# Optimization experiments

Hardware: AMD Instinct MI355X
Metric: run time of the kernel (lower is better)

Reference implementation:

```python
import jax, jax.numpy as jnp
import numpy as np

LEVEL_SHAPES = ((100, 100), (50, 50), (25, 25))  # (H, W) per feature level
B, S, D, H, L, P, FFN = 2, 13125, 256, 8, 3, 4, 1024
Dh = D // H


def setup_inputs() -> dict:
    key = jax.random.key(0)
    ks = jax.random.split(key, 24)

    def rn(k, shape, s=0.02):
        return jax.random.normal(k, shape, jnp.float32) * s

    starts = np.cumsum([0] + [h * w for h, w in LEVEL_SHAPES])[:-1]
    return {
        "x": jax.random.normal(ks[0], (B, S, D), jnp.float32),
        "pos_embed": jax.random.normal(ks[1], (B, S, D), jnp.float32) * 0.1,
        "ref_points": jax.random.uniform(ks[2], (B, S, L, 2), jnp.float32),
        "W_off": rn(ks[3], (D, H * L * P * 2)),
        "b_off": rn(ks[4], (H * L * P * 2,), 0.5),
        "W_attn": rn(ks[5], (D, H * L * P)),
        "b_attn": rn(ks[6], (H * L * P,)),
        "W_val": rn(ks[7], (D, D)),
        "b_val": rn(ks[8], (D,)),
        "W_out": rn(ks[9], (D, D)),
        "b_out": rn(ks[10], (D,)),
        "g1": jnp.ones((D,), jnp.float32),
        "be1": jnp.zeros((D,), jnp.float32),
        "W1": rn(ks[11], (D, FFN)),
        "b1": rn(ks[12], (FFN,)),
        "W2": rn(ks[13], (FFN, D)),
        "b2": rn(ks[14], (D,)),
        "g2": jnp.ones((D,), jnp.float32),
        "be2": jnp.zeros((D,), jnp.float32),
        "level_shapes": jnp.array(LEVEL_SHAPES, jnp.int32),
        "level_start_idx": jnp.array(starts, jnp.int32),
    }


def layer_norm(x, g, b, eps=1e-5):
    m = jnp.mean(x, -1, keepdims=True)
    v = jnp.var(x, -1, keepdims=True)
    return (x - m) * jax.lax.rsqrt(v + eps) * g + b


def bilinear_sample(vl, loc, Hl, Wl):
    # vl: [B,H,S_l,Dh]; loc: [B,H,S,P,2] normalized (x,y) in [0,1]
    # grid_sample semantics: align_corners=False, padding_mode='zeros'
    x = loc[..., 0] * Wl - 0.5
    y = loc[..., 1] * Hl - 0.5
    x0 = jnp.floor(x)
    y0 = jnp.floor(y)
    fx = x - x0
    fy = y - y0
    x0i = x0.astype(jnp.int32)
    y0i = y0.astype(jnp.int32)
    out = 0.0
    for dy, dx, w in ((0, 0, (1 - fx) * (1 - fy)), (0, 1, fx * (1 - fy)),
                      (1, 0, (1 - fx) * fy), (1, 1, fx * fy)):
        xi = x0i + dx
        yi = y0i + dy
        valid = (xi >= 0) & (xi < Wl) & (yi >= 0) & (yi < Hl)
        idx = jnp.clip(yi, 0, Hl - 1) * Wl + jnp.clip(xi, 0, Wl - 1)
        b_, h_, s_, p_ = idx.shape
        g = jnp.take_along_axis(vl, idx.reshape(b_, h_, s_ * p_)[..., None], axis=2)
        g = g.reshape(b_, h_, s_, p_, Dh)
        out = out + g * (w * valid)[..., None]
    return out  # [B,H,S,P,Dh]


def ms_deform_attn(q, x, ref_points, W_off, b_off, W_attn, b_attn, W_val, b_val, W_out, b_out):
    value = (x @ W_val + b_val).reshape(B, S, H, Dh).transpose(0, 2, 1, 3)  # [B,H,S,Dh]
    off = (q @ W_off + b_off).reshape(B, S, H, L, P, 2)
    attn = jax.nn.softmax((q @ W_attn + b_attn).reshape(B, S, H, L * P), axis=-1)
    attn = attn.reshape(B, S, H, L, P).transpose(0, 2, 1, 3, 4)  # [B,H,S,L,P]
    # offset normalizer is (W, H) per level
    norm = jnp.array([[w, h] for h, w in LEVEL_SHAPES], jnp.float32)
    loc = ref_points[:, :, None, :, None, :] + off / norm[None, None, None, :, None, :]
    loc = loc.transpose(0, 2, 1, 3, 4, 5)  # [B,H,S,L,P,2]
    s0 = 0
    sampled = []
    for l, (Hl, Wl) in enumerate(LEVEL_SHAPES):
        vl = jax.lax.slice_in_dim(value, s0, s0 + Hl * Wl, axis=2)
        sampled.append(bilinear_sample(vl, loc[:, :, :, l], Hl, Wl))
        s0 += Hl * Wl
    sampled = jnp.stack(sampled, axis=3)  # [B,H,S,L,P,Dh]
    out = jnp.einsum('bhslp,bhslpd->bshd', attn, sampled).reshape(B, S, D)
    return out @ W_out + b_out


def reference(x, pos_embed, ref_points, W_off, b_off, W_attn, b_attn, W_val, b_val,
              W_out, b_out, g1, be1, W1, b1, W2, b2, g2, be2,
              level_shapes, level_start_idx):
    q = x + pos_embed
    attn_out = ms_deform_attn(q, x, ref_points, W_off, b_off, W_attn, b_attn,
                              W_val, b_val, W_out, b_out)
    h1 = layer_norm(x + attn_out, g1, be1)
    ffn = jax.nn.relu(h1 @ W1 + b1) @ W2 + b2
    return layer_norm(h1 + ffn, g2, be2)
```

## Files before the change

### kernel.cpp

```cpp
#include <hip/hip_runtime.h>
#include <hip/hip_bf16.h>

namespace {

constexpr int kB = 2, kS = 13125, kD = 256, kH = 8, kL = 3, kP = 4, kFFN = 1024, kDh = 32;
constexpr int kM = kB * kS;

typedef __attribute__((ext_vector_type(8))) short short8v;
typedef __attribute__((ext_vector_type(4))) float f32x4;
typedef __attribute__((ext_vector_type(2))) float f32x2;
typedef __attribute__((ext_vector_type(2))) unsigned int uint2v;

__device__ __forceinline__ float bf2f(unsigned short u) {
  unsigned int x = ((unsigned int)u) << 16;
  return __builtin_bit_cast(float, x);
}
__device__ __forceinline__ unsigned short f2bf(float f) {
  unsigned int u = __builtin_bit_cast(unsigned int, f);
  u += 0x7FFFu + ((u >> 16) & 1u);
  return (unsigned short)(u >> 16);
}

__device__ __forceinline__ void gload_lds16(const void* g, void* l) {
  __builtin_amdgcn_global_load_lds(
      (const __attribute__((address_space(1))) unsigned int*)g,
      (__attribute__((address_space(3))) unsigned int*)l, 16, 0, 0);
}

__global__ __launch_bounds__(256) void wprep_kernel(const float* __restrict__ W,
                                                    unsigned short* __restrict__ Wt,
                                                    int K, int N, int total) {
  int idx = blockIdx.x * 256 + threadIdx.x;
  if (idx >= total) return;
  int n = idx / K, k = idx - n * K;
  float v = (n < N) ? W[(size_t)k * N + n] : 0.f;
  Wt[idx] = f2bf(v);
}

__global__ __launch_bounds__(256) void wprep_comb(const float* __restrict__ Woff,
                                                  const float* __restrict__ Wattn,
                                                  const float* __restrict__ boff,
                                                  const float* __restrict__ battn,
                                                  unsigned short* __restrict__ Wt,
                                                  float* __restrict__ bc) {
  int idx = blockIdx.x * 256 + threadIdx.x;
  if (idx >= 288 * 256) return;
  int n = idx >> 8, k = idx & 255;
  int h = n / 36, j = n - h * 36;
  float v = (j < 24) ? Woff[(size_t)k * 192 + h * 24 + j]
                     : Wattn[(size_t)k * 96 + h * 12 + (j - 24)];
  Wt[idx] = f2bf(v);
  if (idx < 288) {
    int hh = idx / 36, jj = idx - hh * 36;
    bc[idx] = (jj < 24) ? boff[hh * 24 + jj] : battn[hh * 12 + (jj - 24)];
  }
}

__global__ __launch_bounds__(256) void prep_kernel(const float4* __restrict__ x,
                                                   const float4* __restrict__ pos,
                                                   ushort4* __restrict__ xb,
                                                   ushort4* __restrict__ qb, int n4) {
  int i = blockIdx.x * 256 + threadIdx.x;
  if (i < n4) {
    float4 a = x[i], b = pos[i];
    xb[i] = make_ushort4(f2bf(a.x), f2bf(a.y), f2bf(a.z), f2bf(a.w));
    qb[i] = make_ushort4(f2bf(a.x + b.x), f2bf(a.y + b.y),
                         f2bf(a.z + b.z), f2bf(a.w + b.w));
  }
}

template <int EPI, bool OBF, int MI, bool VHM>
__global__ __launch_bounds__(256) void mfma_gemm(const unsigned short* __restrict__ A,
                                                 const unsigned short* __restrict__ Bt,
                                                 const float* __restrict__ bias,
                                                 void* __restrict__ Cp,
                                                 int M, int N, int K) {
  constexpr int BM = MI * 32;
  __shared__ unsigned short smem[2 * 128 * 32];
  unsigned short* As = smem;
  unsigned short* Bs = smem + BM * 32;
  const int tid = threadIdx.x;
  const int w = tid >> 6, lane = tid & 63;
  const int m0 = blockIdx.y * BM, n0 = blockIdx.x * 128;
  const int wr = w >> 1, wc = w & 1;
  const int r_ = lane >> 2, sl = lane & 3;

  f32x4 acc[MI][4] = {};

  for (int k0 = 0; k0 < K; k0 += 32) {
#pragma unroll
    for (int i = 0; i < MI / 2; ++i) {
      const int row = i * 64 + w * 16 + r_;
      const int sg = sl ^ ((row >> 1) & 3);
      int arow = m0 + row;
      arow = arow < M ? arow : M - 1;
      gload_lds16(A + (size_t)arow * K + k0 + sg * 8, &As[(i * 64 + w * 16) * 32]);
    }
#pragma unroll
    for (int i = 0; i < 2; ++i) {
      const int row = i * 64 + w * 16 + r_;
      const int sg = sl ^ ((row >> 1) & 3);
      gload_lds16(Bt + (size_t)(n0 + row) * K + k0 + sg * 8, &Bs[(i * 64 + w * 16) * 32]);
    }
    __syncthreads();
    short8v a[MI], b[4];
#pragma unroll
    for (int mi = 0; mi < MI; ++mi) {
      const int row = wr * (MI * 16) + mi * 16 + (lane & 15);
      const int slot = (lane >> 4) ^ ((row >> 1) & 3);
      a[mi] = *(const short8v*)&As[row * 32 + slot * 8];
    }
#pragma unroll
    for (int ni = 0; ni < 4; ++ni) {
      const int row = wc * 64 + ni * 16 + (lane & 15);
      const int slot = (lane >> 4) ^ ((row >> 1) & 3);
      b[ni] = *(const short8v*)&Bs[row * 32 + slot * 8];
    }
#pragma unroll
    for (int mi = 0; mi < MI; ++mi)
#pragma unroll
      for (int ni = 0; ni < 4; ++ni)
        acc[mi][ni] = __builtin_amdgcn_mfma_f32_16x16x32_bf16(a[mi], b[ni], acc[mi][ni], 0, 0, 0);
    __syncthreads();
  }

  const int cr = lane >> 4, cc = lane & 15;
  if (OBF) {
    unsigned short* Cs = smem;
#pragma unroll
    for (int half = 0; half < MI / 2; ++half) {
      if (MI == 2 || wr == half) {
#pragma unroll
        for (int ni = 0; ni < 4; ++ni) {
          const int col = wc * 64 + ni * 16 + cc;
          const float bv = bias[n0 + col];
#pragma unroll
          for (int mi = 0; mi < MI; ++mi)
#pragma unroll
            for (int r = 0; r < 4; ++r) {
              const int loc = wr * (MI * 16) + mi * 16 + cr * 4 + r - half * 64;
              float v = acc[mi][ni][r] + bv;
              if (EPI == 2) v = fmaxf(v, 0.f);
              const int ch = (col >> 3) ^ (loc & 7);
              Cs[loc * 128 + ch * 8 + (col & 7)] = f2bf(v);
            }
        }
      }
      __syncthreads();
      const int lr = tid >> 4, lc = tid & 15;
#pragma unroll
      for (int pp = 0; pp < 4; ++pp) {
        const int loc = pp * 16 + lr;
        const int grow = m0 + half * 64 + loc;
        const short8v vv = *(const short8v*)&Cs[loc * 128 + ((lc ^ (loc & 7)) * 8)];
        if (grow < M) {
          if (VHM) {
            const int col = n0 + lc * 8;
            const int bb = grow >= kS ? 1 : 0;
            const int ss = grow - bb * kS;
            const int hh = col >> 5;
            *(short8v*)((unsigned short*)Cp +
                        (((size_t)(bb * kH + hh) * kS + ss) * kDh + (col & 31))) = vv;
          } else {
            *(short8v*)((unsigned short*)Cp + (size_t)grow * N + n0 + lc * 8) = vv;
          }
        }
      }
      __syncthreads();
    }
  } else {
#pragma unroll
    for (int ni = 0; ni < 4; ++ni) {
      const int col = n0 + wc * 64 + ni * 16 + cc;
      if (col >= N) continue;
      const float bv = bias[col];
#pragma unroll
      for (int mi = 0; mi < MI; ++mi) {
#pragma unroll
        for (int r = 0; r < 4; ++r) {
          const int row = m0 + wr * (MI * 16) + mi * 16 + cr * 4 + r;
          if (row >= M) continue;
          ((float*)Cp)[(size_t)row * N + col] = acc[mi][ni][r] + bv;
        }
      }
    }
  }
}

__global__ __launch_bounds__(256) void ffn_fused(const unsigned short* __restrict__ Ain,
                                                 const unsigned short* __restrict__ W1t,
                                                 const unsigned short* __restrict__ W2t,
                                                 const float* __restrict__ b1,
                                                 const float* __restrict__ b2,
                                                 unsigned short* __restrict__ Cp,
                                                 int M) {
  __shared__ unsigned short W1s[2][64 * 256];
  __shared__ unsigned short Ps[2 * 64 * 32];
  const int tid = threadIdx.x;
  const int w = tid >> 6, lane = tid & 63;
  const int m0 = blockIdx.x * 64;
  const int cr = lane >> 4, cc = lane & 15;

  short8v areg[8];
  {
    int grow = m0 + w * 16 + cc;
    grow = grow < M ? grow : M - 1;
    const unsigned short* ap = Ain + (size_t)grow * 256 + cr * 8;
#pragma unroll
    for (int kk = 0; kk < 8; ++kk) areg[kk] = *(const short8v*)(ap + kk * 32);
  }

  auto stage_w1 = [&](int jt, int buf) {
    const unsigned short* src = W1t + (size_t)jt * 64 * 256;
#pragma unroll
    for (int it = 0; it < 8; ++it) {
      const int idx = it * 256 + tid;
      const int kk = idx >> 8;
      const int row = (idx >> 2) & 63;
      const int sl = idx & 3;
      const int ssl = sl ^ ((row >> 1) & 3);
      gload_lds16(src + (size_t)row * 256 + kk * 32 + ssl * 8, &W1s[buf][idx * 8]);
    }
  };

  f32x4 acc[4][4] = {};

  stage_w1(0, 0);
  __syncthreads();

  for (int jt = 0; jt < 16; ++jt) {
    const int buf = jt & 1;
    if (jt < 15) stage_w1(jt + 1, buf ^ 1);

    f32x4 p1[4] = {};
#pragma unroll
    for (int kk = 0; kk < 8; ++kk) {
#pragma unroll
      for (int ni = 0; ni < 4; ++ni) {
        const int row = ni * 16 + cc;
        const short8v wv = *(const short8v*)
            &W1s[buf][kk * 2048 + row * 32 + ((cr ^ ((row >> 1) & 3)) * 8)];
        p1[ni] = __builtin_amdgcn_mfma_f32_16x16x32_bf16(wv, areg[kk], p1[ni], 0, 0, 0);
      }
    }
    {
      const int row = w * 16 + cc;
      const int rsw = (row >> 1) & 3;
#pragma unroll
      for (int ni = 0; ni < 4; ++ni) {
        const float4 bv = *(const float4*)&b1[jt * 64 + ni * 16 + cr * 4];
        const unsigned int u0 =
            (unsigned)f2bf(fmaxf(p1[ni][0] + bv.x, 0.f)) |
            ((unsigned)f2bf(fmaxf(p1[ni][1] + bv.y, 0.f)) << 16);
        const unsigned int u1 =
            (unsigned)f2bf(fmaxf(p1[ni][2] + bv.z, 0.f)) |
            ((unsigned)f2bf(fmaxf(p1[ni][3] + bv.w, 0.f)) << 16);
        const int kb = ni >> 1;
        const int slot = (ni & 1) * 2 + (cr >> 1);
        uint2v* dst = (uint2v*)&Ps[kb * 2048 + row * 32 + ((slot ^ rsw) * 8) + (cr & 1) * 4];
        *dst = (uint2v){u0, u1};
      }
    }
    __syncthreads();

#pragma unroll
    for (int kk2 = 0; kk2 < 2; ++kk2) {
      short8v pf[4];
#pragma unroll
      for (int mi = 0; mi < 4; ++mi) {
        const int row = mi * 16 + cc;
        pf[mi] = *(const short8v*)
            &Ps[kk2 * 2048 + row * 32 + ((cr ^ ((row >> 1) & 3)) * 8)];
      }
#pragma unroll
      for (int ni = 0; ni < 4; ++ni) {
        const int ncol = w * 64 + ni * 16 + cc;
        const short8v wv = *(const short8v*)(W2t + (size_t)ncol * 1024 + jt * 64 + kk2 * 32 + cr * 8);
#pragma unroll
        for (int mi = 0; mi < 4; ++mi)
          acc[mi][ni] = __builtin_amdgcn_mfma_f32_16x16x32_bf16(pf[mi], wv, acc[mi][ni], 0, 0, 0);
      }
    }
    __syncthreads();
  }

  unsigned short* Cs = &W1s[0][0];
#pragma unroll
  for (int ni = 0; ni < 4; ++ni) {
    const int col = w * 64 + ni * 16 + cc;
    const float bv = b2[col];
#pragma unroll
    for (int mi = 0; mi < 4; ++mi)
#pragma unroll
      for (int r = 0; r < 4; ++r) {
        const int row = mi * 16 + cr * 4 + r;
        const float v = acc[mi][ni][r] + bv;
        Cs[row * 256 + (((col >> 3) ^ (row & 7)) * 8) + (col & 7)] = f2bf(v);
      }
  }
  __syncthreads();
#pragma unroll
  for (int it = 0; it < 8; ++it) {
    const int row = it * 8 + (tid >> 5);
    const int grow = m0 + row;
    const int ch = tid & 31;
    const short8v vv = *(const short8v*)&Cs[row * 256 + ((ch ^ (row & 7)) * 8)];
    if (grow < M) *(short8v*)(Cp + (size_t)grow * 256 + ch * 8) = vv;
  }
}

__device__ __forceinline__ void acc2u(f32x2* acc, unsigned u, int i, float m) {
  f32x2 v;
  v.x = __builtin_bit_cast(float, u << 16);
  v.y = __builtin_bit_cast(float, u & 0xFFFF0000u);
  acc[i] += m * v;
}
__device__ __forceinline__ void acc_corner(f32x2* acc, uint4 q, float m) {
  acc2u(acc, q.x, 0, m);
  acc2u(acc, q.y, 1, m);
  acc2u(acc, q.z, 2, m);
  acc2u(acc, q.w, 3, m);
}

__global__ __launch_bounds__(256) void sample_kernel(const unsigned short* __restrict__ value,
                                                     const float* __restrict__ oa,
                                                     const float* __restrict__ refp,
                                                     unsigned short* __restrict__ out) {
  const int tid = threadIdx.x;
  const int sub = tid >> 2;
  const int lane = tid & 3;
  const int gi = blockIdx.x * 64 + sub;
  if (gi >= kB * kS * kH) return;
  const int h = gi & 7;
  const int bs = gi >> 3;
  const int b = (bs >= kS) ? 1 : 0;

  const float* op = oa + (size_t)bs * 288 + h * 36;
  const float* al = op + 24;
  float w[12];
  float mx = -1e30f;
#pragma unroll
  for (int i = 0; i < 12; ++i) { w[i] = al[i]; mx = fmaxf(mx, w[i]); }
  float sum = 0.f;
#pragma unroll
  for (int i = 0; i < 12; ++i) { w[i] = __expf(w[i] - mx); sum += w[i]; }
  const float inv = 1.f / sum;
#pragma unroll
  for (int i = 0; i < 12; ++i) w[i] *= inv;

  const float* rp = refp + (size_t)bs * (kL * 2);
  const unsigned short* vbase = value + ((size_t)(b * kH + h) * kS) * kDh + lane * 8;

  const int LH[3] = {100, 50, 25}, LW[3] = {100, 50, 25}, LS[3] = {0, 10000, 12500};
  f32x2 acc[4] = {};
#pragma unroll
  for (int l = 0; l < 3; ++l) {
    const int Wi = LW[l], Hi = LH[l];
    const float Wl = (float)Wi, Hl = (float)Hi;
    const float rxw = rp[l * 2 + 0] * Wl - 0.5f;
    const float ryh = rp[l * 2 + 1] * Hl - 0.5f;
    const unsigned short* lvl = vbase + (size_t)LS[l] * kDh;
#pragma unroll
    for (int p = 0; p < 4; ++p) {
      const float ox = op[l * 8 + p * 2 + 0], oy = op[l * 8 + p * 2 + 1];
      const float xf = rxw + ox;
      const float yf = ryh + oy;
      const float x0f = floorf(xf), y0f = floorf(yf);
      const float fx = xf - x0f, fy = yf - y0f;
      const int x0 = (int)x0f, y0 = (int)y0f;
      const int x1 = x0 + 1, y1 = y0 + 1;
      const bool vx0 = (unsigned)x0 < (unsigned)Wi;
      const bool vx1 = (unsigned)x1 < (unsigned)Wi;
      const bool vy0 = (unsigned)y0 < (unsigned)Hi;
      const bool vy1 = (unsigned)y1 < (unsigned)Hi;
      const int cx0 = min(max(x0, 0), Wi - 1), cx1 = min(max(x1, 0), Wi - 1);
      const int cy0 = min(max(y0, 0), Hi - 1), cy1 = min(max(y1, 0), Hi - 1);
      const float aw = w[l * 4 + p];
      const float ax = aw * fx, a0 = aw - ax;
      const float w00 = a0 - a0 * fy, w10 = a0 * fy;
      const float w01 = ax - ax * fy, w11 = ax * fy;
      const float m00 = (vx0 && vy0) ? w00 : 0.f;
      const float m01 = (vx1 && vy0) ? w01 : 0.f;
      const float m10 = (vx0 && vy1) ? w10 : 0.f;
      const float m11 = (vx1 && vy1) ? w11 : 0.f;
      const int ry0 = cy0 * Wi, ry1 = cy1 * Wi;
      const uint4 q00 = *(const uint4*)(lvl + (size_t)(ry0 + cx0) * kDh);
      const uint4 q01 = *(const uint4*)(lvl + (size_t)(ry0 + cx1) * kDh);
      const uint4 q10 = *(const uint4*)(lvl + (size_t)(ry1 + cx0) * kDh);
      const uint4 q11 = *(const uint4*)(lvl + (size_t)(ry1 + cx1) * kDh);
      acc_corner(acc, q00, m00);
      acc_corner(acc, q01, m01);
      acc_corner(acc, q10, m10);
      acc_corner(acc, q11, m11);
    }
  }
  unsigned short r[8];
#pragma unroll
  for (int i = 0; i < 4; ++i) {
    r[2 * i] = f2bf(acc[i].x);
    r[2 * i + 1] = f2bf(acc[i].y);
  }
  *(short8v*)(out + (size_t)bs * kD + h * kDh + lane * 8) = *(const short8v*)r;
}

template <int WB>
__global__ __launch_bounds__(256) void lnres_kernel(const float* __restrict__ X,
                                                    const unsigned short* __restrict__ Ab,
                                                    const float* __restrict__ g,
                                                    const float* __restrict__ be,
                                                    float* __restrict__ out,
                                                    unsigned short* __restrict__ outb,
                                                    int rows) {
  const int wid = threadIdx.x >> 6, lane = threadIdx.x & 63;
  const int row = blockIdx.x * 4 + wid;
  if (row >= rows) return;
  const float4 v = ((const float4*)(X + (size_t)row * kD))[lane];
  const ushort4 a4 = ((const ushort4*)(Ab + (size_t)row * kD))[lane];
  float4 t;
  t.x = v.x + bf2f(a4.x);
  t.y = v.y + bf2f(a4.y);
  t.z = v.z + bf2f(a4.z);
  t.w = v.w + bf2f(a4.w);
  float s = t.x + t.y + t.z + t.w;
  float sq = t.x * t.x + t.y * t.y + t.z * t.z + t.w * t.w;
#pragma unroll
  for (int o = 1; o < 64; o <<= 1) {
    s += __shfl_xor(s, o);
    sq += __shfl_xor(sq, o);
  }
  const float mean = s * (1.f / kD);
  const float var = sq * (1.f / kD) - mean * mean;
  const float rs = rsqrtf(var + 1e-5f);
  const float4 gg = ((const float4*)g)[lane];
  const float4 bb = ((const float4*)be)[lane];
  float4 o4;
  o4.x = (t.x - mean) * rs * gg.x + bb.x;
  o4.y = (t.y - mean) * rs * gg.y + bb.y;
  o4.z = (t.z - mean) * rs * gg.z + bb.z;
  o4.w = (t.w - mean) * rs * gg.w + bb.w;
  ((float4*)(out + (size_t)row * kD))[lane] = o4;
  if (WB) {
    ((ushort4*)(outb + (size_t)row * kD))[lane] =
        make_ushort4(f2bf(o4.x), f2bf(o4.y), f2bf(o4.z), f2bf(o4.w));
  }
}

}

extern "C" void kernel_launch(void* const* d_in, const int* in_sizes, int n_in,
                              void* d_out, int out_size, void* d_ws, size_t ws_size,
                              hipStream_t stream) {
  const float* x      = (const float*)d_in[0];
  const float* pos    = (const float*)d_in[1];
  const float* refp   = (const float*)d_in[2];
  const float* W_off  = (const float*)d_in[3];
  const float* b_off  = (const float*)d_in[4];
  const float* W_attn = (const float*)d_in[5];
  const float* b_attn = (const float*)d_in[6];
  const float* W_val  = (const float*)d_in[7];
  const float* b_val  = (const float*)d_in[8];
  const float* W_out  = (const float*)d_in[9];
  const float* b_out  = (const float*)d_in[10];
  const float* g1     = (const float*)d_in[11];
  const float* be1    = (const float*)d_in[12];
  const float* W1     = (const float*)d_in[13];
  const float* b1     = (const float*)d_in[14];
  const float* W2     = (const float*)d_in[15];
  const float* b2     = (const float*)d_in[16];
  const float* g2     = (const float*)d_in[17];
  const float* be2    = (const float*)d_in[18];
  float* outp = (float*)d_out;

  char* ws = (char*)d_ws;
  unsigned short* Wvt = (unsigned short*)(ws + 0);
  unsigned short* Wot = (unsigned short*)(ws + 131072);
  unsigned short* Wct = (unsigned short*)(ws + 262144);
  float* bcomb        = (float*)(ws + 262144 + 288 * 512);
  unsigned short* W1t = (unsigned short*)(ws + 458752);
  unsigned short* W2t = (unsigned short*)(ws + 983040);
  const size_t MDb = (size_t)kM * kD * 2;
  char* regA = ws + 1507328;
  char* regB = regA + MDb;
  char* regC = regB + MDb;
  char* regG = regC + 43680000;

  unsigned short* xb    = (unsigned short*)regA;
  unsigned short* aob   = (unsigned short*)regA;
  unsigned short* qb    = (unsigned short*)regB;
  unsigned short* f2b   = (unsigned short*)regB;
  unsigned short* value = (unsigned short*)regC;
  float* oa   = (float*)(regC + MDb);
  float* h1   = (float*)regC;
  unsigned short* h1b = (unsigned short*)(regC + (size_t)kM * kD * 4);
  unsigned short* sv  = (unsigned short*)regG;

  const dim3 blk(256);
  const int mt64 = (kM + 63) / 64;
  const int n4 = kM * kD / 4;

  wprep_kernel<<<(256 * 256 + 255) / 256, blk, 0, stream>>>(W_val, Wvt, 256, 256, 256 * 256);
  wprep_kernel<<<(256 * 256 + 255) / 256, blk, 0, stream>>>(W_out, Wot, 256, 256, 256 * 256);
  wprep_comb<<<288, blk, 0, stream>>>(W_off, W_attn, b_off, b_attn, Wct, bcomb);
  wprep_kernel<<<(1024 * 256 + 255) / 256, blk, 0, stream>>>(W1, W1t, 256, 1024, 1024 * 256);
  wprep_kernel<<<(256 * 1024 + 255) / 256, blk, 0, stream>>>(W2, W2t, 1024, 256, 256 * 1024);

  prep_kernel<<<(n4 + 255) / 256, blk, 0, stream>>>((const float4*)x, (const float4*)pos,
                                                    (ushort4*)xb, (ushort4*)qb, n4);
  mfma_gemm<0, true, 2, true><<<dim3(2, mt64), blk, 0, stream>>>(xb, Wvt, b_val, value,
                                                                 kM, 256, 256);
  mfma_gemm<0, false, 2, false><<<dim3(3, mt64), blk, 0, stream>>>(qb, Wct, bcomb, oa,
                                                                   kM, 288, 256);
  sample_kernel<<<(kB * kS * kH + 63) / 64, blk, 0, stream>>>(value, oa, refp, sv);
  mfma_gemm<0, true, 2, false><<<dim3(2, mt64), blk, 0, stream>>>(sv, Wot, b_out, aob,
                                                                  kM, 256, 256);
  lnres_kernel<1><<<(kM + 3) / 4, blk, 0, stream>>>(x, aob, g1, be1, h1, h1b, kM);
  ffn_fused<<<mt64, blk, 0, stream>>>(h1b, W1t, W2t, b1, b2, f2b, kM);
  lnres_kernel<0><<<(kM + 3) / 4, blk, 0, stream>>>(h1, f2b, g2, be2, outp, nullptr, kM);
}
```

Baseline: 204.1 us.

## Read W1 directly from global in fused FFN, shrink LDS to raise occupancy

Drops the double-buffered 64KB LDS staging of W1 tiles and has each wave load W1 fragments straight from global/L2 memory. The P (hidden activation) buffer is double-buffered, which allows one of the two barriers per iteration to be removed, and the output staging is done in two 128-column halves to fit the smaller LDS. The aim is to cut LDS use enough for several blocks per CU and to reduce synchronisation. The cost is redundant global loads of W1 by every wave and block, which depend on cache hits.

```diff
diff --git a/kernel.cpp b/kernel.cpp
--- a/kernel.cpp
+++ b/kernel.cpp
@@ -194,8 +194,7 @@
                                                  const float* __restrict__ b2,
                                                  unsigned short* __restrict__ Cp,
                                                  int M) {
-  __shared__ unsigned short W1s[2][64 * 256];
-  __shared__ unsigned short Ps[2 * 64 * 32];
+  __shared__ unsigned short Ps[2][2 * 64 * 32];
   const int tid = threadIdx.x;
   const int w = tid >> 6, lane = tid & 63;
   const int m0 = blockIdx.x * 64;
@@ -210,40 +209,22 @@
     for (int kk = 0; kk < 8; ++kk) areg[kk] = *(const short8v*)(ap + kk * 32);
   }
 
-  auto stage_w1 = [&](int jt, int buf) {
-    const unsigned short* src = W1t + (size_t)jt * 64 * 256;
-#pragma unroll
-    for (int it = 0; it < 8; ++it) {
-      const int idx = it * 256 + tid;
-      const int kk = idx >> 8;
-      const int row = (idx >> 2) & 63;
-      const int sl = idx & 3;
-      const int ssl = sl ^ ((row >> 1) & 3);
-      gload_lds16(src + (size_t)row * 256 + kk * 32 + ssl * 8, &W1s[buf][idx * 8]);
-    }
-  };
-
   f32x4 acc[4][4] = {};
 
-  stage_w1(0, 0);
-  __syncthreads();
-
   for (int jt = 0; jt < 16; ++jt) {
-    const int buf = jt & 1;
-    if (jt < 15) stage_w1(jt + 1, buf ^ 1);
-
+    const unsigned short* w1p = W1t + (size_t)jt * 64 * 256;
     f32x4 p1[4] = {};
 #pragma unroll
     for (int kk = 0; kk < 8; ++kk) {
 #pragma unroll
       for (int ni = 0; ni < 4; ++ni) {
-        const int row = ni * 16 + cc;
-        const short8v wv = *(const short8v*)
-            &W1s[buf][kk * 2048 + row * 32 + ((cr ^ ((row >> 1) & 3)) * 8)];
+        const short8v wv =
+            *(const short8v*)(w1p + (size_t)(ni * 16 + cc) * 256 + kk * 32 + cr * 8);
         p1[ni] = __builtin_amdgcn_mfma_f32_16x16x32_bf16(wv, areg[kk], p1[ni], 0, 0, 0);
       }
     }
     {
+      unsigned short* P = Ps[jt & 1];
       const int row = w * 16 + cc;
       const int rsw = (row >> 1) & 3;
 #pragma unroll
@@ -257,12 +238,16 @@
             ((unsigned)f2bf(fmaxf(p1[ni][3] + bv.w, 0.f)) << 16);
         const int kb = ni >> 1;
         const int slot = (ni & 1) * 2 + (cr >> 1);
-        uint2v* dst = (uint2v*)&Ps[kb * 2048 + row * 32 + ((slot ^ rsw) * 8) + (cr & 1) * 4];
+        uint2v* dst = (uint2v*)&P[kb * 2048 + row * 32 + ((slot ^ rsw) * 8) + (cr & 1) * 4];
         *dst = (uint2v){u0, u1};
       }
     }
-    __syncthreads();
-
+    asm volatile("s_waitcnt lgkmcnt(0)" ::: "memory");
+    __builtin_amdgcn_sched_barrier(0);
+    __builtin_amdgcn_s_barrier();
+    __builtin_amdgcn_sched_barrier(0);
+
+    const unsigned short* Pr = Ps[jt & 1];
 #pragma unroll
     for (int kk2 = 0; kk2 < 2; ++kk2) {
       short8v pf[4];
@@ -270,42 +255,50 @@
       for (int mi = 0; mi < 4; ++mi) {
         const int row = mi * 16 + cc;
         pf[mi] = *(const short8v*)
-            &Ps[kk2 * 2048 + row * 32 + ((cr ^ ((row >> 1) & 3)) * 8)];
+            &Pr[kk2 * 2048 + row * 32 + ((cr ^ ((row >> 1) & 3)) * 8)];
       }
 #pragma unroll
       for (int ni = 0; ni < 4; ++ni) {
         const int ncol = w * 64 + ni * 16 + cc;
-        const short8v wv = *(const short8v*)(W2t + (size_t)ncol * 1024 + jt * 64 + kk2 * 32 + cr * 8);
+        const short8v wv =
+            *(const short8v*)(W2t + (size_t)ncol * 1024 + jt * 64 + kk2 * 32 + cr * 8);
 #pragma unroll
         for (int mi = 0; mi < 4; ++mi)
           acc[mi][ni] = __builtin_amdgcn_mfma_f32_16x16x32_bf16(pf[mi], wv, acc[mi][ni], 0, 0, 0);
       }
     }
+  }
+
+  asm volatile("s_waitcnt lgkmcnt(0)" ::: "memory");
+  __builtin_amdgcn_s_barrier();
+  unsigned short* Cs = &Ps[0][0];
+#pragma unroll
+  for (int half = 0; half < 2; ++half) {
+    if ((w >> 1) == half) {
+#pragma unroll
+      for (int ni = 0; ni < 4; ++ni) {
+        const int col = (w & 1) * 64 + ni * 16 + cc;
+        const float bv = b2[half * 128 + col];
+#pragma unroll
+        for (int mi = 0; mi < 4; ++mi)
+#pragma unroll
+          for (int r = 0; r < 4; ++r) {
+            const int loc = mi * 16 + cr * 4 + r;
+            const float v = acc[mi][ni][r] + bv;
+            Cs[loc * 128 + (((col >> 3) ^ (loc & 7)) * 8) + (col & 7)] = f2bf(v);
+          }
+      }
+    }
     __syncthreads();
-  }
-
-  unsigned short* Cs = &W1s[0][0];
-#pragma unroll
-  for (int ni = 0; ni < 4; ++ni) {
-    const int col = w * 64 + ni * 16 + cc;
-    const float bv = b2[col];
-#pragma unroll
-    for (int mi = 0; mi < 4; ++mi)
-#pragma unroll
-      for (int r = 0; r < 4; ++r) {
-        const int row = mi * 16 + cr * 4 + r;
-        const float v = acc[mi][ni][r] + bv;
-        Cs[row * 256 + (((col >> 3) ^ (row & 7)) * 8) + (col & 7)] = f2bf(v);
-      }
-  }
-  __syncthreads();
-#pragma unroll
-  for (int it = 0; it < 8; ++it) {
-    const int row = it * 8 + (tid >> 5);
-    const int grow = m0 + row;
-    const int ch = tid & 31;
-    const short8v vv = *(const short8v*)&Cs[row * 256 + ((ch ^ (row & 7)) * 8)];
-    if (grow < M) *(short8v*)(Cp + (size_t)grow * 256 + ch * 8) = vv;
+    const int lr = tid >> 4, lc = tid & 15;
+#pragma unroll
+    for (int pp = 0; pp < 4; ++pp) {
+      const int loc = pp * 16 + lr;
+      const int grow = m0 + loc;
+      const short8v vv = *(const short8v*)&Cs[loc * 128 + ((lc ^ (loc & 7)) * 8)];
+      if (grow < M) *(short8v*)(Cp + (size_t)grow * 256 + half * 128 + lc * 8) = vv;
+    }
+    __syncthreads();
   }
 }
 
```

Result: slower. 304.8 us (+49.3%).

## Split fused FFN block across eight waves instead of four

Applied to the files above, without the earlier changes.

The fused FFN kernel now launches 512 threads per 64-row tile instead of 256. In the first GEMM the waves split the hidden chunk by halves, and in the second they split the output columns into 32-wide slices. Per-wave accumulators and MFMA counts are halved, which is meant to cut register pressure and add latency hiding within each block. In exchange, each A fragment is loaded twice across waves and more waves contend at the barriers.

```diff
diff --git a/kernel.cpp b/kernel.cpp
--- a/kernel.cpp
+++ b/kernel.cpp
@@ -187,23 +187,25 @@
   }
 }
 
-__global__ __launch_bounds__(256) void ffn_fused(const unsigned short* __restrict__ Ain,
-                                                 const unsigned short* __restrict__ W1t,
-                                                 const unsigned short* __restrict__ W2t,
-                                                 const float* __restrict__ b1,
-                                                 const float* __restrict__ b2,
-                                                 unsigned short* __restrict__ Cp,
-                                                 int M) {
+__global__ __launch_bounds__(512, 4) void ffn_fused(const unsigned short* __restrict__ Ain,
+                                                    const unsigned short* __restrict__ W1t,
+                                                    const unsigned short* __restrict__ W2t,
+                                                    const float* __restrict__ b1,
+                                                    const float* __restrict__ b2,
+                                                    unsigned short* __restrict__ Cp,
+                                                    int M) {
   __shared__ unsigned short W1s[2][64 * 256];
   __shared__ unsigned short Ps[2 * 64 * 32];
   const int tid = threadIdx.x;
   const int w = tid >> 6, lane = tid & 63;
   const int m0 = blockIdx.x * 64;
   const int cr = lane >> 4, cc = lane & 15;
+  const int mw = w & 3;
+  const int fw = w >> 2;
 
   short8v areg[8];
   {
-    int grow = m0 + w * 16 + cc;
+    int grow = m0 + mw * 16 + cc;
     grow = grow < M ? grow : M - 1;
     const unsigned short* ap = Ain + (size_t)grow * 256 + cr * 8;
 #pragma unroll
@@ -213,8 +215,8 @@
   auto stage_w1 = [&](int jt, int buf) {
     const unsigned short* src = W1t + (size_t)jt * 64 * 256;
 #pragma unroll
-    for (int it = 0; it < 8; ++it) {
-      const int idx = it * 256 + tid;
+    for (int it = 0; it < 4; ++it) {
+      const int idx = it * 512 + tid;
       const int kk = idx >> 8;
       const int row = (idx >> 2) & 63;
       const int sl = idx & 3;
@@ -223,7 +225,7 @@
     }
   };
 
-  f32x4 acc[4][4] = {};
+  f32x4 acc[4][2] = {};
 
   stage_w1(0, 0);
   __syncthreads();
@@ -232,32 +234,31 @@
     const int buf = jt & 1;
     if (jt < 15) stage_w1(jt + 1, buf ^ 1);
 
-    f32x4 p1[4] = {};
+    f32x4 p1[2] = {};
 #pragma unroll
     for (int kk = 0; kk < 8; ++kk) {
 #pragma unroll
-      for (int ni = 0; ni < 4; ++ni) {
-        const int row = ni * 16 + cc;
+      for (int lf = 0; lf < 2; ++lf) {
+        const int row = fw * 32 + lf * 16 + cc;
         const short8v wv = *(const short8v*)
             &W1s[buf][kk * 2048 + row * 32 + ((cr ^ ((row >> 1) & 3)) * 8)];
-        p1[ni] = __builtin_amdgcn_mfma_f32_16x16x32_bf16(wv, areg[kk], p1[ni], 0, 0, 0);
+        p1[lf] = __builtin_amdgcn_mfma_f32_16x16x32_bf16(wv, areg[kk], p1[lf], 0, 0, 0);
       }
     }
     {
-      const int row = w * 16 + cc;
+      const int row = mw * 16 + cc;
       const int rsw = (row >> 1) & 3;
 #pragma unroll
-      for (int ni = 0; ni < 4; ++ni) {
-        const float4 bv = *(const float4*)&b1[jt * 64 + ni * 16 + cr * 4];
+      for (int lf = 0; lf < 2; ++lf) {
+        const float4 bv = *(const float4*)&b1[jt * 64 + fw * 32 + lf * 16 + cr * 4];
         const unsigned int u0 =
-            (unsigned)f2bf(fmaxf(p1[ni][0] + bv.x, 0.f)) |
-            ((unsigned)f2bf(fmaxf(p1[ni][1] + bv.y, 0.f)) << 16);
+            (unsigned)f2bf(fmaxf(p1[lf][0] + bv.x, 0.f)) |
+            ((unsigned)f2bf(fmaxf(p1[lf][1] + bv.y, 0.f)) << 16);
         const unsigned int u1 =
-            (unsigned)f2bf(fmaxf(p1[ni][2] + bv.z, 0.f)) |
-            ((unsigned)f2bf(fmaxf(p1[ni][3] + bv.w, 0.f)) << 16);
-        const int kb = ni >> 1;
-        const int slot = (ni & 1) * 2 + (cr >> 1);
-        uint2v* dst = (uint2v*)&Ps[kb * 2048 + row * 32 + ((slot ^ rsw) * 8) + (cr & 1) * 4];
+            (unsigned)f2bf(fmaxf(p1[lf][2] + bv.z, 0.f)) |
+            ((unsigned)f2bf(fmaxf(p1[lf][3] + bv.w, 0.f)) << 16);
+        const int slot = lf * 2 + (cr >> 1);
+        uint2v* dst = (uint2v*)&Ps[fw * 2048 + row * 32 + ((slot ^ rsw) * 8) + (cr & 1) * 4];
         *dst = (uint2v){u0, u1};
       }
     }
@@ -273,9 +274,10 @@
             &Ps[kk2 * 2048 + row * 32 + ((cr ^ ((row >> 1) & 3)) * 8)];
       }
 #pragma unroll
-      for (int ni = 0; ni < 4; ++ni) {
-        const int ncol = w * 64 + ni * 16 + cc;
-        const short8v wv = *(const short8v*)(W2t + (size_t)ncol * 1024 + jt * 64 + kk2 * 32 + cr * 8);
+      for (int ni = 0; ni < 2; ++ni) {
+        const int ncol = w * 32 + ni * 16 + cc;
+        const short8v wv =
+            *(const short8v*)(W2t + (size_t)ncol * 1024 + jt * 64 + kk2 * 32 + cr * 8);
 #pragma unroll
         for (int mi = 0; mi < 4; ++mi)
           acc[mi][ni] = __builtin_amdgcn_mfma_f32_16x16x32_bf16(pf[mi], wv, acc[mi][ni], 0, 0, 0);
@@ -286,8 +288,8 @@
 
   unsigned short* Cs = &W1s[0][0];
 #pragma unroll
-  for (int ni = 0; ni < 4; ++ni) {
-    const int col = w * 64 + ni * 16 + cc;
+  for (int ni = 0; ni < 2; ++ni) {
+    const int col = w * 32 + ni * 16 + cc;
     const float bv = b2[col];
 #pragma unroll
     for (int mi = 0; mi < 4; ++mi)
@@ -300,8 +302,8 @@
   }
   __syncthreads();
 #pragma unroll
-  for (int it = 0; it < 8; ++it) {
-    const int row = it * 8 + (tid >> 5);
+  for (int it = 0; it < 4; ++it) {
+    const int row = it * 16 + (tid >> 5);
     const int grow = m0 + row;
     const int ch = tid & 31;
     const short8v vv = *(const short8v*)&Cs[row * 256 + ((ch ^ (row & 7)) * 8)];
@@ -514,6 +516,6 @@
   mfma_gemm<0, true, 2, false><<<dim3(2, mt64), blk, 0, stream>>>(sv, Wot, b_out, aob,
                                                                   kM, 256, 256);
   lnres_kernel<1><<<(kM + 3) / 4, blk, 0, stream>>>(x, aob, g1, be1, h1, h1b, kM);
-  ffn_fused<<<mt64, blk, 0, stream>>>(h1b, W1t, W2t, b1, b2, f2b, kM);
+  ffn_fused<<<mt64, dim3(512), 0, stream>>>(h1b, W1t, W2t, b1, b2, f2b, kM);
   lnres_kernel<0><<<(kM + 3) / 4, blk, 0, stream>>>(h1, f2b, g2, be2, outp, nullptr, kM);
 }
```

Result: no change. 206.7 us (+1.3%).
